# Performance work log

Measured on AMD Instinct MI355X. Metric: run time of the kernel, lower is better.

## Reference

```python
import jax, jax.numpy as jnp
import numpy as np


def setup_inputs() -> dict:
    key = jax.random.key(0)
    k1, = jax.random.split(key, 1)
    x = jax.random.normal(k1, (16, 512, 64, 64), dtype=jnp.float32)
    gamma = jnp.zeros((1,), dtype=jnp.float32)
    return {"x": x, "gamma": gamma}


def reference(x, gamma):
    B, C, H, W = x.shape
    q = x.reshape(B, C, H * W)              # B x C x N
    # energy: B x C x C  (channel-channel gram matrix)
    energy = jnp.einsum('bcn,bdn->bcd', q, q)
    # max-subtract transform: max over last dim minus energy
    energy_new = jnp.max(energy, axis=-1, keepdims=True) - energy
    attention = jax.nn.softmax(energy_new, axis=-1)  # B x C x C
    out = jnp.einsum('bcd,bdn->bcn', attention, q).reshape(B, C, H, W)
    return gamma * out + x
```

## Files before the change

kernel.cpp:

```cpp
#include <hip/hip_runtime.h>
#include <hip/hip_bf16.h>
#include <stdint.h>

#define B_ 16
#define C_ 512
#define N_ 4096
#define KS_ 4

typedef float f32x4 __attribute__((ext_vector_type(4)));
typedef __bf16 bf16x8 __attribute__((ext_vector_type(8)));

static __device__ __forceinline__ unsigned short f2bf(float f) {
    unsigned int u = __float_as_uint(f);
    u += 0x7fffu + ((u >> 16) & 1u);
    return (unsigned short)(u >> 16);
}

static __device__ __forceinline__ void gload_lds16(const void* g, void* l) {
    __builtin_amdgcn_global_load_lds(
        (__attribute__((address_space(1))) unsigned int*)(g),
        (__attribute__((address_space(3))) unsigned int*)(l),
        16, 0, 0);
}

__global__ __launch_bounds__(256)
void convert_transpose(const float* __restrict__ x,
                       unsigned short* __restrict__ q16,
                       unsigned short* __restrict__ qt16) {
    __shared__ unsigned short tile[64][65];
    int b  = blockIdx.z;
    int c0 = blockIdx.y * 64, n0 = blockIdx.x * 64;
    int tx = threadIdx.x & 15, ty = threadIdx.x >> 4;

    const float*    xb  = x    + ((size_t)b * C_ + c0) * N_ + n0;
    unsigned short* qb  = q16  + ((size_t)b * C_ + c0) * N_ + n0;
    unsigned short* qtb = qt16 + ((size_t)b * N_ + n0) * C_ + c0;

#pragma unroll
    for (int s = 0; s < 4; ++s) {
        int rr = s * 16 + ty;
        float4 v = *(const float4*)(xb + (size_t)rr * N_ + tx * 4);
        unsigned short h0 = f2bf(v.x), h1 = f2bf(v.y), h2 = f2bf(v.z), h3 = f2bf(v.w);
        tile[rr][tx * 4 + 0] = h0;
        tile[rr][tx * 4 + 1] = h1;
        tile[rr][tx * 4 + 2] = h2;
        tile[rr][tx * 4 + 3] = h3;
        ushort4 p; p.x = h0; p.y = h1; p.z = h2; p.w = h3;
        *(ushort4*)(qb + (size_t)rr * N_ + tx * 4) = p;
    }
    __syncthreads();
#pragma unroll
    for (int s = 0; s < 4; ++s) {
        int nr = s * 16 + ty;
        ushort4 p;
        p.x = tile[tx * 4 + 0][nr];
        p.y = tile[tx * 4 + 1][nr];
        p.z = tile[tx * 4 + 2][nr];
        p.w = tile[tx * 4 + 3][nr];
        *(ushort4*)(qtb + (size_t)nr * C_ + tx * 4) = p;
    }
}

__global__ __launch_bounds__(256)
void gemm_gram_splitk(const unsigned short* __restrict__ q16,
                      float* __restrict__ epart) {
    int bz = blockIdx.z;
    int b = bz >> 2, ks = bz & 3;
    const int Kc = N_ / KS_;
    const char* Qb = (const char*)(q16 + (size_t)b * C_ * N_) + (size_t)ks * Kc * 2;
    const int row_bytes = N_ * 2;
    int m0 = blockIdx.y * 128, n0 = blockIdx.x * 128;

    __shared__ unsigned short As[128 * 32];
    __shared__ unsigned short Bs[128 * 32];

    int t = threadIdx.x;
    int lane = t & 63, wave = t >> 6;
    int wm = (wave >> 1) * 64, wn = (wave & 1) * 64;
    int qd = lane >> 4, r = lane & 15;

    f32x4 acc[4][4] = {};

    for (int k0 = 0; k0 < Kc; k0 += 32) {
        __syncthreads();
#pragma unroll
        for (int i = 0; i < 2; ++i) {
            int o = (i * 256 + t) * 16;
            int mrow = o >> 6, inrow = o & 63;
            gload_lds16(Qb + (size_t)(m0 + mrow) * row_bytes + k0 * 2 + inrow,
                        (char*)As + o);
            gload_lds16(Qb + (size_t)(n0 + mrow) * row_bytes + k0 * 2 + inrow,
                        (char*)Bs + o);
        }
        __syncthreads();

        bf16x8 af[4], bfr[4];
#pragma unroll
        for (int i = 0; i < 4; ++i)
            af[i] = *(const bf16x8*)&As[(wm + i * 16 + r) * 32 + qd * 8];
#pragma unroll
        for (int j = 0; j < 4; ++j)
            bfr[j] = *(const bf16x8*)&Bs[(wn + j * 16 + r) * 32 + qd * 8];
#pragma unroll
        for (int i = 0; i < 4; ++i)
#pragma unroll
            for (int j = 0; j < 4; ++j)
                acc[i][j] = __builtin_amdgcn_mfma_f32_16x16x32_bf16(af[i], bfr[j], acc[i][j], 0, 0, 0);
    }

    float* Db = epart + (size_t)(ks * B_ + b) * C_ * C_;
#pragma unroll
    for (int i = 0; i < 4; ++i)
#pragma unroll
        for (int j = 0; j < 4; ++j) {
            int cbase = m0 + wm + i * 16 + qd * 4;
            int d     = n0 + wn + j * 16 + r;
            *(f32x4*)(Db + (size_t)d * C_ + cbase) = acc[i][j];
        }
}

__global__ __launch_bounds__(256)
void softmax_neg4(const float* __restrict__ epart, unsigned short* __restrict__ att) {
    size_t row = blockIdx.x;
    const size_t slice = (size_t)B_ * C_ * C_;
    const float* e = epart + row * C_;
    int t = threadIdx.x;

    float e0 = 0.f, e1 = 0.f;
#pragma unroll
    for (int s = 0; s < KS_; ++s) {
        e0 += e[s * slice + t];
        e1 += e[s * slice + t + 256];
    }
    float m = fminf(e0, e1);
#pragma unroll
    for (int off = 32; off > 0; off >>= 1) m = fminf(m, __shfl_down(m, off, 64));
    __shared__ float red[8];
    if ((t & 63) == 0) red[t >> 6] = m;
    __syncthreads();
    m = fminf(fminf(red[0], red[1]), fminf(red[2], red[3]));

    float p0 = __expf(m - e0), p1 = __expf(m - e1);
    float s = p0 + p1;
#pragma unroll
    for (int off = 32; off > 0; off >>= 1) s += __shfl_down(s, off, 64);
    if ((t & 63) == 0) red[4 + (t >> 6)] = s;
    __syncthreads();
    s = red[4] + red[5] + red[6] + red[7];
    float inv = 1.0f / s;

    att[row * C_ + t]       = f2bf(p0 * inv);
    att[row * C_ + t + 256] = f2bf(p1 * inv);
}

__global__ __launch_bounds__(256)
void gemm_out_t(const unsigned short* __restrict__ att,
                const unsigned short* __restrict__ qt16,
                const float* __restrict__ x,
                const float* __restrict__ gamma,
                float* __restrict__ y) {
    const int K = C_;
    int b = blockIdx.z;
    const unsigned short* Ab = qt16 + (size_t)b * N_ * C_;
    const unsigned short* Bb = att  + (size_t)b * C_ * C_;
    int m0 = blockIdx.x * 128;
    int n0 = blockIdx.y * 128;

    __shared__ unsigned short As[128 * 32];
    __shared__ unsigned short Bs[128 * 32];

    int t = threadIdx.x;
    int lane = t & 63, wave = t >> 6;
    int wm = (wave >> 1) * 64, wn = (wave & 1) * 64;
    int qd = lane >> 4, r = lane & 15;

    f32x4 acc[4][4] = {};

    for (int k0 = 0; k0 < K; k0 += 32) {
        __syncthreads();
#pragma unroll
        for (int i = 0; i < 2; ++i) {
            int o = (i * 256 + t) * 16;
            int mrow = o >> 6, inrow = o & 63;
            gload_lds16((const char*)Ab + (size_t)(m0 + mrow) * (K * 2) + k0 * 2 + inrow,
                        (char*)As + o);
            gload_lds16((const char*)Bb + (size_t)(n0 + mrow) * (K * 2) + k0 * 2 + inrow,
                        (char*)Bs + o);
        }
        __syncthreads();

        bf16x8 af[4], bfr[4];
#pragma unroll
        for (int i = 0; i < 4; ++i)
            af[i] = *(const bf16x8*)&As[(wm + i * 16 + r) * 32 + qd * 8];
#pragma unroll
        for (int j = 0; j < 4; ++j)
            bfr[j] = *(const bf16x8*)&Bs[(wn + j * 16 + r) * 32 + qd * 8];
#pragma unroll
        for (int i = 0; i < 4; ++i)
#pragma unroll
            for (int j = 0; j < 4; ++j)
                acc[i][j] = __builtin_amdgcn_mfma_f32_16x16x32_bf16(af[i], bfr[j], acc[i][j], 0, 0, 0);
    }

    float g = gamma[0];
    const float* xb = x + (size_t)b * C_ * N_;
    float*       yb = y + (size_t)b * C_ * N_;
#pragma unroll
    for (int i = 0; i < 4; ++i)
#pragma unroll
        for (int j = 0; j < 4; ++j) {
            int nbase = m0 + wm + i * 16 + qd * 4;
            int c     = n0 + wn + j * 16 + r;
            size_t idx = (size_t)c * N_ + nbase;
            float4 xv = *(const float4*)(xb + idx);
            f32x4 a = acc[i][j];
            float4 o;
            o.x = g * a[0] + xv.x;
            o.y = g * a[1] + xv.y;
            o.z = g * a[2] + xv.z;
            o.w = g * a[3] + xv.w;
            *(float4*)(yb + idx) = o;
        }
}

extern "C" void kernel_launch(void* const* d_in, const int* in_sizes, int n_in,
                              void* d_out, int out_size, void* d_ws, size_t ws_size,
                              hipStream_t stream) {
    const float* x     = (const float*)d_in[0];
    const float* gamma = (const float*)d_in[1];
    float*       y     = (float*)d_out;

    char* ws = (char*)d_ws;
    unsigned short* q16   = (unsigned short*)(ws);
    unsigned short* qt16  = (unsigned short*)(ws + 67108864);
    unsigned short* att16 = (unsigned short*)(ws + 134217728);
    float*          epart = (float*)d_out;

    convert_transpose<<<dim3(N_ / 64, C_ / 64, B_), dim3(256), 0, stream>>>(x, q16, qt16);
    gemm_gram_splitk<<<dim3(C_ / 128, C_ / 128, B_ * KS_), dim3(256), 0, stream>>>(q16, epart);
    softmax_neg4<<<dim3(B_ * C_), dim3(256), 0, stream>>>(epart, att16);
    gemm_out_t<<<dim3(N_ / 128, C_ / 128, B_), dim3(256), 0, stream>>>(att16, qt16, x, gamma, y);
}
```

Baseline: 420.9 us.

## Shrink GEMM N-tiles, reorder block mapping, register-only convert transpose

```diff
diff --git a/kernel.cpp b/kernel.cpp
--- a/kernel.cpp
+++ b/kernel.cpp
@@ -1,5 +1,4 @@
 #include <hip/hip_runtime.h>
-#include <hip/hip_bf16.h>
 #include <stdint.h>
 
 #define B_ 16
@@ -27,84 +26,81 @@
 void convert_transpose(const float* __restrict__ x,
                        unsigned short* __restrict__ q16,
                        unsigned short* __restrict__ qt16) {
-    __shared__ unsigned short tile[64][65];
     int b  = blockIdx.z;
-    int c0 = blockIdx.y * 64, n0 = blockIdx.x * 64;
-    int tx = threadIdx.x & 15, ty = threadIdx.x >> 4;
-
-    const float*    xb  = x    + ((size_t)b * C_ + c0) * N_ + n0;
-    unsigned short* qb  = q16  + ((size_t)b * C_ + c0) * N_ + n0;
-    unsigned short* qtb = qt16 + ((size_t)b * N_ + n0) * C_ + c0;
-
-#pragma unroll
-    for (int s = 0; s < 4; ++s) {
-        int rr = s * 16 + ty;
-        float4 v = *(const float4*)(xb + (size_t)rr * N_ + tx * 4);
-        unsigned short h0 = f2bf(v.x), h1 = f2bf(v.y), h2 = f2bf(v.z), h3 = f2bf(v.w);
-        tile[rr][tx * 4 + 0] = h0;
-        tile[rr][tx * 4 + 1] = h1;
-        tile[rr][tx * 4 + 2] = h2;
-        tile[rr][tx * 4 + 3] = h3;
-        ushort4 p; p.x = h0; p.y = h1; p.z = h2; p.w = h3;
-        *(ushort4*)(qb + (size_t)rr * N_ + tx * 4) = p;
-    }
-    __syncthreads();
-#pragma unroll
-    for (int s = 0; s < 4; ++s) {
-        int nr = s * 16 + ty;
-        ushort4 p;
-        p.x = tile[tx * 4 + 0][nr];
-        p.y = tile[tx * 4 + 1][nr];
-        p.z = tile[tx * 4 + 2][nr];
-        p.w = tile[tx * 4 + 3][nr];
-        *(ushort4*)(qtb + (size_t)nr * C_ + tx * 4) = p;
-    }
-}
-
-__global__ __launch_bounds__(256)
+    int n0 = blockIdx.x * 64  + (threadIdx.x & 15) * 4;
+    int c0 = blockIdx.y * 128 + (threadIdx.x >> 4) * 8;
+
+    const float*    xb  = x   + (size_t)b * C_ * N_;
+    unsigned short* qb  = q16 + (size_t)b * C_ * N_;
+    unsigned short* qtb = qt16 + (size_t)b * N_ * C_;
+
+    unsigned short hv[8][4];
+#pragma unroll
+    for (int cc = 0; cc < 8; ++cc) {
+        float4 v = *(const float4*)(xb + (size_t)(c0 + cc) * N_ + n0);
+        hv[cc][0] = f2bf(v.x); hv[cc][1] = f2bf(v.y);
+        hv[cc][2] = f2bf(v.z); hv[cc][3] = f2bf(v.w);
+        ushort4 p; p.x = hv[cc][0]; p.y = hv[cc][1]; p.z = hv[cc][2]; p.w = hv[cc][3];
+        *(ushort4*)(qb + (size_t)(c0 + cc) * N_ + n0) = p;
+    }
+#pragma unroll
+    for (int nn = 0; nn < 4; ++nn) {
+        unsigned short hh[8];
+#pragma unroll
+        for (int cc = 0; cc < 8; ++cc) hh[cc] = hv[cc][nn];
+        *(uint4*)(qtb + (size_t)(n0 + nn) * C_ + c0) = *(uint4*)hh;
+    }
+}
+
+__global__ __launch_bounds__(256, 6)
 void gemm_gram_splitk(const unsigned short* __restrict__ q16,
                       float* __restrict__ epart) {
-    int bz = blockIdx.z;
-    int b = bz >> 2, ks = bz & 3;
+    int bid   = blockIdx.x;
+    int slice = bid & 63;
+    int b = slice >> 2, ks = slice & 3;
+    int tile = bid >> 6;
+    int n0 = (tile & 7) * 64;
+    int m0 = (tile >> 3) * 128;
+
     const int Kc = N_ / KS_;
     const char* Qb = (const char*)(q16 + (size_t)b * C_ * N_) + (size_t)ks * Kc * 2;
     const int row_bytes = N_ * 2;
-    int m0 = blockIdx.y * 128, n0 = blockIdx.x * 128;
 
     __shared__ unsigned short As[128 * 32];
-    __shared__ unsigned short Bs[128 * 32];
+    __shared__ unsigned short Bs[64 * 32];
 
     int t = threadIdx.x;
     int lane = t & 63, wave = t >> 6;
-    int wm = (wave >> 1) * 64, wn = (wave & 1) * 64;
+    int wm = (wave >> 1) * 64, wn = (wave & 1) * 32;
     int qd = lane >> 4, r = lane & 15;
 
-    f32x4 acc[4][4] = {};
+    f32x4 acc[4][2] = {};
 
     for (int k0 = 0; k0 < Kc; k0 += 32) {
         __syncthreads();
-#pragma unroll
-        for (int i = 0; i < 2; ++i) {
-            int o = (i * 256 + t) * 16;
-            int mrow = o >> 6, inrow = o & 63;
-            gload_lds16(Qb + (size_t)(m0 + mrow) * row_bytes + k0 * 2 + inrow,
+        {
+            int o = t * 16;
+            gload_lds16(Qb + (size_t)(m0 + (o >> 6)) * row_bytes + k0 * 2 + (o & 63),
                         (char*)As + o);
-            gload_lds16(Qb + (size_t)(n0 + mrow) * row_bytes + k0 * 2 + inrow,
+            int o2 = o + 4096;
+            gload_lds16(Qb + (size_t)(m0 + (o2 >> 6)) * row_bytes + k0 * 2 + (o2 & 63),
+                        (char*)As + o2);
+            gload_lds16(Qb + (size_t)(n0 + (o >> 6)) * row_bytes + k0 * 2 + (o & 63),
                         (char*)Bs + o);
         }
         __syncthreads();
 
-        bf16x8 af[4], bfr[4];
+        bf16x8 af[4], bfr[2];
 #pragma unroll
         for (int i = 0; i < 4; ++i)
             af[i] = *(const bf16x8*)&As[(wm + i * 16 + r) * 32 + qd * 8];
 #pragma unroll
-        for (int j = 0; j < 4; ++j)
+        for (int j = 0; j < 2; ++j)
             bfr[j] = *(const bf16x8*)&Bs[(wn + j * 16 + r) * 32 + qd * 8];
 #pragma unroll
         for (int i = 0; i < 4; ++i)
 #pragma unroll
-            for (int j = 0; j < 4; ++j)
+            for (int j = 0; j < 2; ++j)
                 acc[i][j] = __builtin_amdgcn_mfma_f32_16x16x32_bf16(af[i], bfr[j], acc[i][j], 0, 0, 0);
     }
 
@@ -112,7 +108,7 @@
 #pragma unroll
     for (int i = 0; i < 4; ++i)
 #pragma unroll
-        for (int j = 0; j < 4; ++j) {
+        for (int j = 0; j < 2; ++j) {
             int cbase = m0 + wm + i * 16 + qd * 4;
             int d     = n0 + wn + j * 16 + r;
             *(f32x4*)(Db + (size_t)d * C_ + cbase) = acc[i][j];
@@ -153,53 +149,58 @@
     att[row * C_ + t + 256] = f2bf(p1 * inv);
 }
 
-__global__ __launch_bounds__(256)
+__global__ __launch_bounds__(256, 6)
 void gemm_out_t(const unsigned short* __restrict__ att,
                 const unsigned short* __restrict__ qt16,
                 const float* __restrict__ x,
                 const float* __restrict__ gamma,
                 float* __restrict__ y) {
     const int K = C_;
-    int b = blockIdx.z;
-    const unsigned short* Ab = qt16 + (size_t)b * N_ * C_;
-    const unsigned short* Bb = att  + (size_t)b * C_ * C_;
-    int m0 = blockIdx.x * 128;
-    int n0 = blockIdx.y * 128;
+    int bid  = blockIdx.x;
+    int b    = bid & 15;
+    int tile = bid >> 4;
+    int m0 = (tile & 31) * 128;
+    int n0 = (tile >> 5) * 64;
+
+    const char* Ab = (const char*)(qt16 + (size_t)b * N_ * C_);
+    const char* Bb = (const char*)(att  + (size_t)b * C_ * C_);
+    const int row_bytes = C_ * 2;
 
     __shared__ unsigned short As[128 * 32];
-    __shared__ unsigned short Bs[128 * 32];
+    __shared__ unsigned short Bs[64 * 32];
 
     int t = threadIdx.x;
     int lane = t & 63, wave = t >> 6;
-    int wm = (wave >> 1) * 64, wn = (wave & 1) * 64;
+    int wm = (wave >> 1) * 64, wn = (wave & 1) * 32;
     int qd = lane >> 4, r = lane & 15;
 
-    f32x4 acc[4][4] = {};
+    f32x4 acc[4][2] = {};
 
     for (int k0 = 0; k0 < K; k0 += 32) {
         __syncthreads();
-#pragma unroll
-        for (int i = 0; i < 2; ++i) {
-            int o = (i * 256 + t) * 16;
-            int mrow = o >> 6, inrow = o & 63;
-            gload_lds16((const char*)Ab + (size_t)(m0 + mrow) * (K * 2) + k0 * 2 + inrow,
+        {
+            int o = t * 16;
+            gload_lds16(Ab + (size_t)(m0 + (o >> 6)) * row_bytes + k0 * 2 + (o & 63),
                         (char*)As + o);
-            gload_lds16((const char*)Bb + (size_t)(n0 + mrow) * (K * 2) + k0 * 2 + inrow,
+            int o2 = o + 4096;
+            gload_lds16(Ab + (size_t)(m0 + (o2 >> 6)) * row_bytes + k0 * 2 + (o2 & 63),
+                        (char*)As + o2);
+            gload_lds16(Bb + (size_t)(n0 + (o >> 6)) * row_bytes + k0 * 2 + (o & 63),
                         (char*)Bs + o);
         }
         __syncthreads();
 
-        bf16x8 af[4], bfr[4];
+        bf16x8 af[4], bfr[2];
 #pragma unroll
         for (int i = 0; i < 4; ++i)
             af[i] = *(const bf16x8*)&As[(wm + i * 16 + r) * 32 + qd * 8];
 #pragma unroll
-        for (int j = 0; j < 4; ++j)
+        for (int j = 0; j < 2; ++j)
             bfr[j] = *(const bf16x8*)&Bs[(wn + j * 16 + r) * 32 + qd * 8];
 #pragma unroll
         for (int i = 0; i < 4; ++i)
 #pragma unroll
-            for (int j = 0; j < 4; ++j)
+            for (int j = 0; j < 2; ++j)
                 acc[i][j] = __builtin_amdgcn_mfma_f32_16x16x32_bf16(af[i], bfr[j], acc[i][j], 0, 0, 0);
     }
 
@@ -209,7 +210,7 @@
 #pragma unroll
     for (int i = 0; i < 4; ++i)
 #pragma unroll
-        for (int j = 0; j < 4; ++j) {
+        for (int j = 0; j < 2; ++j) {
             int nbase = m0 + wm + i * 16 + qd * 4;
             int c     = n0 + wn + j * 16 + r;
             size_t idx = (size_t)c * N_ + nbase;
@@ -237,8 +238,8 @@
     unsigned short* att16 = (unsigned short*)(ws + 134217728);
     float*          epart = (float*)d_out;
 
-    convert_transpose<<<dim3(N_ / 64, C_ / 64, B_), dim3(256), 0, stream>>>(x, q16, qt16);
-    gemm_gram_splitk<<<dim3(C_ / 128, C_ / 128, B_ * KS_), dim3(256), 0, stream>>>(q16, epart);
+    convert_transpose<<<dim3(N_ / 64, C_ / 128, B_), dim3(256), 0, stream>>>(x, q16, qt16);
+    gemm_gram_splitk<<<dim3(2048), dim3(256), 0, stream>>>(q16, epart);
     softmax_neg4<<<dim3(B_ * C_), dim3(256), 0, stream>>>(epart, att16);
-    gemm_out_t<<<dim3(N_ / 128, C_ / 128, B_), dim3(256), 0, stream>>>(att16, qt16, x, gamma, y);
-}
+    gemm_out_t<<<dim3(4096), dim3(256), 0, stream>>>(att16, qt16, x, gamma, y);
+}
```

After: 440.4 us. +4.6%, slower.
